# Kernel tuning notes

Hardware: AMD Instinct MI355X
Metric: run time of the kernel (lower is better)

Reference implementation:

```python
import jax, jax.numpy as jnp
import numpy as np

N, M, D = 16384, 8192, 3
ATOM_DIMS, CHEM, K = 6, 16, 16
GAMMA = 1.0
BIG = 1e10


def _leaky(x):
    return jax.nn.leaky_relu(x, negative_slope=0.2)


def _linear(x, W, b=None):
    # torch nn.Linear: y = x @ W.T + b, W: [out, in]
    y = x @ W.T
    return y if b is None else y + b


def setup_inputs() -> dict:
    key = jax.random.key(0)
    ks = jax.random.split(key, 16)

    def lin(k, out_d, in_d):
        bound = 1.0 / np.sqrt(in_d)
        k1, k2 = jax.random.split(k)
        W = jax.random.uniform(k1, (out_d, in_d), minval=-bound, maxval=bound, dtype=jnp.float32)
        b = jax.random.uniform(k2, (out_d,), minval=-bound, maxval=bound, dtype=jnp.float32)
        return W, b

    W_t1, b_t1 = lin(ks[0], CHEM, ATOM_DIMS)
    W_t2, b_t2 = lin(ks[1], CHEM, CHEM)
    W_t3, b_t3 = lin(ks[2], CHEM, CHEM)
    W_att = jax.random.uniform(ks[3], (1, K), minval=-1.0 / np.sqrt(K), maxval=1.0 / np.sqrt(K), dtype=jnp.float32)
    W_e1, b_e1 = lin(ks[4], CHEM, CHEM)
    W_e2, b_e2 = lin(ks[5], CHEM, CHEM)
    W_e3, b_e3 = lin(ks[6], CHEM, CHEM)

    return {
        "xyz": jax.random.normal(ks[7], (N, D), dtype=jnp.float32) * 10.0,
        "atom_xyz": jax.random.normal(ks[8], (M, D), dtype=jnp.float32) * 10.0,
        "atomtypes": jax.random.uniform(ks[9], (M, ATOM_DIMS), dtype=jnp.float32),
        "batch": jnp.zeros((N,), dtype=jnp.int64),
        "atom_batch": jnp.zeros((M,), dtype=jnp.int64),
        "W_t1": W_t1, "b_t1": b_t1, "W_t2": W_t2, "b_t2": b_t2, "W_t3": W_t3, "b_t3": b_t3,
        "W_att": W_att,
        "W_e1": W_e1, "b_e1": b_e1, "W_e2": W_e2, "b_e2": b_e2, "W_e3": W_e3, "b_e3": b_e3,
    }


def reference(xyz, atom_xyz, atomtypes, batch, atom_batch,
              W_t1, b_t1, W_t2, b_t2, W_t3, b_t3, W_att,
              W_e1, b_e1, W_e2, b_e2, W_e3, b_e3):
    # transform_types MLP on atom one-hots -> [M, CHEM]
    t = atomtypes[:, :ATOM_DIMS]
    t = _leaky(_linear(t, W_t1, b_t1))
    t = _leaky(_linear(t, W_t2, b_t2))
    t = _leaky(_linear(t, W_t3, b_t3))

    # batched kNN: squared distances [N, M], cross-batch pairs masked out
    d2 = (jnp.sum(xyz * xyz, -1)[:, None] + jnp.sum(atom_xyz * atom_xyz, -1)[None, :]
          - 2.0 * (xyz @ atom_xyz.T))
    d2 = jnp.where(batch[:, None] == atom_batch[None, :], d2, BIG)
    _, idx = jax.lax.top_k(-d2, K)  # idx: [N, K] nearest atoms

    x_ik = atom_xyz[idx]                       # [N, K, 3]
    vecs = xyz[:, None, :] - x_ik              # [N, K, 3]
    dists = jnp.sum(vecs * vecs, -1)           # [N, K]
    w = jnp.power(dists + 1e-8, -(1.0 + GAMMA) / 2.0)
    norm_vec = vecs * w[:, :, None]            # [N, K, 3]
    feat = t[idx]                              # [N, K, CHEM]

    # outer product [N, K, 3, C] transposed to [N, C, 3, K], attention Linear over K,
    # fused into one einsum (dropout is identity at eval)
    fx = jnp.einsum('nkd,nkc,k->ncd', norm_vec, feat, W_att[0])  # [N, C, 3]
    fx = jnp.sqrt(jnp.sum(fx * fx, -1))        # [N, C]

    fx = _leaky(_linear(fx, W_e1, b_e1))
    fx = _leaky(_linear(fx, W_e2, b_e2))
    fx = _linear(fx, W_e3, b_e3)
    return fx
```

## Files before the change

kernel.cpp:

```cpp
#include <hip/hip_runtime.h>
#include <cfloat>

#define NPTS   16384
#define MATOMS 8192
#define CH     16
#define ADIM   6
#define KNN    16
#define GROUPS_PER_BLOCK 8
#define BIGF   1e10f
#define SLOTS  16
#define CHUNK  512
#define NCHUNK (MATOMS/CHUNK)
#define VMINC  4
#define NPASS  (VMINC + NCHUNK)

__device__ __forceinline__ float leakyf(float x) { return x >= 0.0f ? x : 0.2f * x; }

__global__ void __launch_bounds__(256) prep_kernel(
    const float* __restrict__ atom_xyz,
    const float* __restrict__ atomtypes,
    const int*   __restrict__ atom_batch,
    const float* __restrict__ Wt1, const float* __restrict__ bt1,
    const float* __restrict__ Wt2, const float* __restrict__ bt2,
    const float* __restrict__ Wt3, const float* __restrict__ bt3,
    float4* __restrict__ pos4,
    float*  __restrict__ tbuf,
    int*    __restrict__ abatch)
{
    __shared__ float w1[CH*ADIM], w2[CH*CH], w3[CH*CH], bb1[CH], bb2[CH], bb3[CH];
    const int tid = threadIdx.x;
    if (tid < CH*ADIM) w1[tid] = Wt1[tid];
    if (tid < CH*CH)   { w2[tid] = Wt2[tid]; w3[tid] = Wt3[tid]; }
    if (tid < CH)      { bb1[tid] = bt1[tid]; bb2[tid] = bt2[tid]; bb3[tid] = bt3[tid]; }
    __syncthreads();
    const int m = blockIdx.x * 256 + tid;
    if (m >= MATOMS) return;

    float x[ADIM];
    #pragma unroll
    for (int j = 0; j < ADIM; ++j) x[j] = atomtypes[m*ADIM + j];

    float h0[CH], h1[CH], h2[CH];
    #pragma unroll
    for (int c = 0; c < CH; ++c) {
        float a = 0.0f;
        #pragma unroll
        for (int j = 0; j < ADIM; ++j) a = fmaf(w1[c*ADIM+j], x[j], a);
        h0[c] = leakyf(a + bb1[c]);
    }
    #pragma unroll
    for (int c = 0; c < CH; ++c) {
        float a = 0.0f;
        #pragma unroll
        for (int j = 0; j < CH; ++j) a = fmaf(w2[c*CH+j], h0[j], a);
        h1[c] = leakyf(a + bb2[c]);
    }
    #pragma unroll
    for (int c = 0; c < CH; ++c) {
        float a = 0.0f;
        #pragma unroll
        for (int j = 0; j < CH; ++j) a = fmaf(w3[c*CH+j], h1[j], a);
        h2[c] = leakyf(a + bb3[c]);
    }
    #pragma unroll
    for (int c = 0; c < CH; ++c) tbuf[m*CH + c] = h2[c];

    const float ax = atom_xyz[m*3+0], ay = atom_xyz[m*3+1], az = atom_xyz[m*3+2];
    const float a2 = __fadd_rn(__fadd_rn(__fmul_rn(ax,ax), __fmul_rn(ay,ay)), __fmul_rn(az,az));
    pos4[m] = make_float4(ax, ay, az, a2);
    abatch[m] = atom_batch[m];
}

__global__ void __launch_bounds__(256) atom_main_kernel(
    const float* __restrict__ xyz,
    const int*   __restrict__ batch,
    const float4* __restrict__ pos4,
    const float* __restrict__ tbuf,
    const int*   __restrict__ abatch,
    const float* __restrict__ Watt,
    const float* __restrict__ We1, const float* __restrict__ be1,
    const float* __restrict__ We2, const float* __restrict__ be2,
    const float* __restrict__ We3, const float* __restrict__ be3,
    float* __restrict__ out)
{
    __shared__ float lw1t[CH*CH], lw2t[CH*CH], lw3t[CH*CH];
    __shared__ float lb1[CH], lb2[CH], lb3[CH], lwatt[KNN];
    __shared__ unsigned short lbuf[GROUPS_PER_BLOCK * SLOTS * 32];
    __shared__ float4 lpos[2][CHUNK];
    __shared__ int    lbat[2][CHUNK];
    const int tid = threadIdx.x;
    lw1t[tid] = We1[(tid & 15)*CH + (tid >> 4)];
    lw2t[tid] = We2[(tid & 15)*CH + (tid >> 4)];
    lw3t[tid] = We3[(tid & 15)*CH + (tid >> 4)];
    if (tid < CH) { lb1[tid] = be1[tid]; lb2[tid] = be2[tid]; lb3[tid] = be3[tid]; lwatt[tid] = Watt[tid]; }

    const int c32 = tid & 31;
    const int grp = tid >> 5;
    const int n   = blockIdx.x * GROUPS_PER_BLOCK + grp;

    const float px = xyz[n*3+0], py = xyz[n*3+1], pz = xyz[n*3+2];
    const float pn2 = __fadd_rn(__fadd_rn(__fmul_rn(px,px), __fmul_rn(py,py)), __fmul_rn(pz,pz));
    const int pb = batch[n];

    {
        const float4 q0 = pos4[tid];
        const float4 q1 = pos4[tid+256];
        const int    e0 = abatch[tid];
        const int    e1 = abatch[tid+256];
        lpos[0][tid] = q0; lpos[0][tid+256] = q1;
        lbat[0][tid] = e0; lbat[0][tid+256] = e1;
    }

    float vmin = FLT_MAX;
    float tauf = 0.0f;
    int   skip = 0;
    int   cnt  = 0;
    unsigned short* seg = &lbuf[grp * (SLOTS*32) + c32];

    for (int g = 0; g < NPASS; ++g) {
        const int cur = g & 1;
        __syncthreads();
        float4 q0, q1; int e0, e1;
        const bool pf = (g+1 < NPASS);
        if (pf) {
            const int nc = (g+1 < VMINC) ? (g+1) : (g+1-VMINC);
            const int base = nc*CHUNK;
            q0 = pos4[base+tid]; q1 = pos4[base+tid+256];
            e0 = abatch[base+tid]; e1 = abatch[base+tid+256];
        }
        if (g == VMINC) {
            float tau = FLT_MAX;
            float v = vmin;
            #pragma unroll
            for (int k = 0; k < KNN; ++k) {
                float d = v;
                d = fminf(d, __shfl_xor(d, 1));
                d = fminf(d, __shfl_xor(d, 2));
                d = fminf(d, __shfl_xor(d, 4));
                d = fminf(d, __shfl_xor(d, 8));
                d = fminf(d, __shfl_xor(d, 16));
                tau = d;
                if (v == d) v = FLT_MAX;
            }
            skip = !(tau < BIGF);
            tauf = tau + (1e-5f*(fabsf(pn2) + fabsf(tau)) + 1e-2f);
        }
        if (g < VMINC) {
            #pragma unroll 4
            for (int t = 0; t < CHUNK/32; ++t) {
                const int il = t*32 + c32;
                const float4 a = lpos[cur][il];
                const float dot = fmaf(pz, a.z, fmaf(py, a.y, __fmul_rn(px, a.x)));
                const float lhs = fmaf(-2.0f, dot, a.w);
                if (lhs < vmin) { if (lbat[cur][il] == pb) vmin = lhs; }
            }
        } else if (!skip) {
            const int cb = g - VMINC;
            #pragma unroll 4
            for (int t = 0; t < CHUNK/32; ++t) {
                const int il = t*32 + c32;
                const float4 a = lpos[cur][il];
                const float dot = fmaf(pz, a.z, fmaf(py, a.y, __fmul_rn(px, a.x)));
                const float lhs = fmaf(-2.0f, dot, a.w);
                if (lhs <= tauf) {
                    if (lbat[cur][il] == pb) {
                        const int gi = cb*CHUNK + il;
                        if (cnt < SLOTS) seg[cnt*32] = (unsigned short)gi;
                        ++cnt;
                    }
                }
            }
        }
        if (pf) {
            lpos[cur^1][tid] = q0; lpos[cur^1][tid+256] = q1;
            lbat[cur^1][tid] = e0; lbat[cur^1][tid+256] = e1;
        }
    }

    int ovf = skip | (cnt > SLOTS);
    ovf |= __shfl_xor(ovf, 1);
    ovf |= __shfl_xor(ovf, 2);
    ovf |= __shfl_xor(ovf, 4);
    ovf |= __shfl_xor(ovf, 8);
    ovf |= __shfl_xor(ovf, 16);

    float bd[KNN]; int bi[KNN];
    #pragma unroll
    for (int j = 0; j < KNN; ++j) { bd[j] = FLT_MAX; bi[j] = 0x7fffffff; }

    if (ovf) {
        for (int t = 0; t < MATOMS/32; ++t) {
            const int i = t*32 + c32;
            const float4 a = pos4[i];
            const int ab = abatch[i];
            const float dot = fmaf(pz, a.z, fmaf(py, a.y, __fmul_rn(px, a.x)));
            float d2 = __fsub_rn(__fadd_rn(pn2, a.w), 2.0f * dot);
            d2 = (ab == pb) ? d2 : BIGF;
            if (d2 < bd[KNN-1]) {
                float d = d2; int id = i;
                #pragma unroll
                for (int j = 0; j < KNN; ++j) {
                    const bool sw = d < bd[j];
                    const float od = bd[j]; const int oi = bi[j];
                    bd[j] = sw ? d  : bd[j];
                    bi[j] = sw ? id : bi[j];
                    d  = sw ? od : d;
                    id = sw ? oi : id;
                }
            }
        }
    } else {
        for (int s = 0; s < cnt; ++s) {
            const int i = (int)seg[s*32];
            const float4 a = pos4[i];
            const float dot = fmaf(pz, a.z, fmaf(py, a.y, __fmul_rn(px, a.x)));
            const float d2 = __fsub_rn(__fadd_rn(pn2, a.w), 2.0f * dot);
            if (d2 < bd[KNN-1]) {
                float d = d2; int id = i;
                #pragma unroll
                for (int j = 0; j < KNN; ++j) {
                    const bool sw = d < bd[j];
                    const float od = bd[j]; const int oi = bi[j];
                    bd[j] = sw ? d  : bd[j];
                    bi[j] = sw ? id : bi[j];
                    d  = sw ? od : d;
                    id = sw ? oi : id;
                }
            }
        }
    }

    int idxk[KNN];
    #pragma unroll
    for (int k = 0; k < KNN; ++k) {
        float d = bd[0]; int i = bi[0];
        #pragma unroll
        for (int m = 1; m <= 16; m <<= 1) {
            const float pd = __shfl_xor(d, m);
            const int   pi = __shfl_xor(i, m);
            const bool take = (pd < d) || (pd == d && pi < i);
            d = take ? pd : d;
            i = take ? pi : i;
        }
        idxk[k] = i;
        const bool win = (bd[0] == d) && (bi[0] == i);
        if (win) {
            #pragma unroll
            for (int j = 0; j < KNN-1; ++j) { bd[j] = bd[j+1]; bi[j] = bi[j+1]; }
            bd[KNN-1] = FLT_MAX; bi[KNN-1] = 0x7fffffff;
        }
    }

    if ((tid & 16) == 0) {
        const int c = tid & 15;
        float ac0 = 0.0f, ac1 = 0.0f, ac2 = 0.0f;
        #pragma unroll
        for (int k = 0; k < KNN; ++k) {
            const int j = idxk[k];
            const float4 a = pos4[j];
            const float v0 = __fsub_rn(px, a.x);
            const float v1 = __fsub_rn(py, a.y);
            const float v2 = __fsub_rn(pz, a.z);
            const float dist = __fadd_rn(__fadd_rn(__fmul_rn(v0,v0), __fmul_rn(v1,v1)), __fmul_rn(v2,v2));
            const float w = 1.0f / __fadd_rn(dist, 1e-8f);
            const float nv0 = __fmul_rn(v0, w);
            const float nv1 = __fmul_rn(v1, w);
            const float nv2 = __fmul_rn(v2, w);
            const float fc = tbuf[(size_t)j * CH + c];
            const float fw = __fmul_rn(fc, lwatt[k]);
            ac0 = fmaf(nv0, fw, ac0);
            ac1 = fmaf(nv1, fw, ac1);
            ac2 = fmaf(nv2, fw, ac2);
        }
        const float s = __fadd_rn(__fadd_rn(__fmul_rn(ac0,ac0), __fmul_rn(ac1,ac1)),
                                  __fmul_rn(ac2,ac2));
        const float fx = sqrtf(s);

        float a1 = 0.0f;
        #pragma unroll
        for (int j = 0; j < CH; ++j) {
            const float fj = __shfl(fx, j, 16);
            a1 = fmaf(lw1t[j*CH + c], fj, a1);
        }
        const float g1 = leakyf(a1 + lb1[c]);

        float a2 = 0.0f;
        #pragma unroll
        for (int j = 0; j < CH; ++j) {
            const float gj = __shfl(g1, j, 16);
            a2 = fmaf(lw2t[j*CH + c], gj, a2);
        }
        const float g2 = leakyf(a2 + lb2[c]);

        float a3 = 0.0f;
        #pragma unroll
        for (int j = 0; j < CH; ++j) {
            const float gj = __shfl(g2, j, 16);
            a3 = fmaf(lw3t[j*CH + c], gj, a3);
        }
        out[(size_t)n*CH + c] = a3 + lb3[c];
    }
}

extern "C" void kernel_launch(void* const* d_in, const int* in_sizes, int n_in,
                              void* d_out, int out_size, void* d_ws, size_t ws_size,
                              hipStream_t stream)
{
    (void)in_sizes; (void)n_in; (void)out_size; (void)ws_size;
    const float* xyz        = (const float*)d_in[0];
    const float* atom_xyz   = (const float*)d_in[1];
    const float* atomtypes  = (const float*)d_in[2];
    const int*   batch      = (const int*)d_in[3];
    const int*   atom_batch = (const int*)d_in[4];
    const float* Wt1 = (const float*)d_in[5];
    const float* bt1 = (const float*)d_in[6];
    const float* Wt2 = (const float*)d_in[7];
    const float* bt2 = (const float*)d_in[8];
    const float* Wt3 = (const float*)d_in[9];
    const float* bt3 = (const float*)d_in[10];
    const float* Watt = (const float*)d_in[11];
    const float* We1 = (const float*)d_in[12];
    const float* be1 = (const float*)d_in[13];
    const float* We2 = (const float*)d_in[14];
    const float* be2 = (const float*)d_in[15];
    const float* We3 = (const float*)d_in[16];
    const float* be3 = (const float*)d_in[17];

    char* ws = (char*)d_ws;
    float4* pos4  = (float4*)ws;
    float*  tbuf  = (float*)(ws + 131072);
    int*    abat  = (int*)(ws + 131072 + 524288);
    float*  out   = (float*)d_out;

    hipLaunchKernelGGL(prep_kernel, dim3(MATOMS/256), dim3(256), 0, stream,
                       atom_xyz, atomtypes, atom_batch,
                       Wt1, bt1, Wt2, bt2, Wt3, bt3,
                       pos4, tbuf, abat);
    hipLaunchKernelGGL(atom_main_kernel, dim3(NPTS/GROUPS_PER_BLOCK), dim3(256), 0, stream,
                       xyz, batch, pos4, tbuf, abat,
                       Watt, We1, be1, We2, be2, We3, be3,
                       out);
}
```

Measured before the change: 132.6 us.

## Sample strided atoms for kNN threshold and share per-group candidate list

The threshold estimate now comes from a strided sample of 1024 atoms read straight from global memory, replacing the four shared-memory warm-up chunks. Candidates under the threshold go into one per-group shared list via shared atomics instead of per-lane 16-slot buffers, and lanes then process that list round-robin. The batch check moves from the scan to the final top-k insertion, which drops the staged batch arrays. This removes passes and shared-memory traffic and balances candidate work across lanes, at the cost of shared atomic contention and a possibly looser threshold, since the list admits candidates from other batches.

```diff
diff --git a/kernel.cpp b/kernel.cpp
--- a/kernel.cpp
+++ b/kernel.cpp
@@ -8,11 +8,9 @@
 #define KNN    16
 #define GROUPS_PER_BLOCK 8
 #define BIGF   1e10f
-#define SLOTS  16
+#define GSLOTS 384
 #define CHUNK  512
 #define NCHUNK (MATOMS/CHUNK)
-#define VMINC  4
-#define NPASS  (VMINC + NCHUNK)
 
 __device__ __forceinline__ float leakyf(float x) { return x >= 0.0f ? x : 0.2f * x; }
 
@@ -85,14 +83,15 @@
 {
     __shared__ float lw1t[CH*CH], lw2t[CH*CH], lw3t[CH*CH];
     __shared__ float lb1[CH], lb2[CH], lb3[CH], lwatt[KNN];
-    __shared__ unsigned short lbuf[GROUPS_PER_BLOCK * SLOTS * 32];
+    __shared__ unsigned short gseg[GROUPS_PER_BLOCK][GSLOTS];
+    __shared__ int gcnt[GROUPS_PER_BLOCK];
     __shared__ float4 lpos[2][CHUNK];
-    __shared__ int    lbat[2][CHUNK];
     const int tid = threadIdx.x;
     lw1t[tid] = We1[(tid & 15)*CH + (tid >> 4)];
     lw2t[tid] = We2[(tid & 15)*CH + (tid >> 4)];
     lw3t[tid] = We3[(tid & 15)*CH + (tid >> 4)];
     if (tid < CH) { lb1[tid] = be1[tid]; lb2[tid] = be2[tid]; lb3[tid] = be3[tid]; lwatt[tid] = Watt[tid]; }
+    if (tid < GROUPS_PER_BLOCK) gcnt[tid] = 0;
 
     const int c32 = tid & 31;
     const int grp = tid >> 5;
@@ -105,57 +104,52 @@
     {
         const float4 q0 = pos4[tid];
         const float4 q1 = pos4[tid+256];
-        const int    e0 = abatch[tid];
-        const int    e1 = abatch[tid+256];
         lpos[0][tid] = q0; lpos[0][tid+256] = q1;
-        lbat[0][tid] = e0; lbat[0][tid+256] = e1;
     }
 
     float vmin = FLT_MAX;
-    float tauf = 0.0f;
-    int   skip = 0;
-    int   cnt  = 0;
-    unsigned short* seg = &lbuf[grp * (SLOTS*32) + c32];
-
-    for (int g = 0; g < NPASS; ++g) {
+    for (int t4 = 0; t4 < 8; ++t4) {
+        float4 A[4];
+        #pragma unroll
+        for (int u = 0; u < 4; ++u) A[u] = pos4[((t4*4 + u)*32 + c32) * 8];
+        #pragma unroll
+        for (int u = 0; u < 4; ++u) {
+            const float dot = fmaf(pz, A[u].z, fmaf(py, A[u].y, __fmul_rn(px, A[u].x)));
+            const float lhs = fmaf(-2.0f, dot, A[u].w);
+            if (lhs < vmin) {
+                if (abatch[((t4*4 + u)*32 + c32) * 8] == pb) vmin = lhs;
+            }
+        }
+    }
+
+    float tau = FLT_MAX;
+    {
+        float v = vmin;
+        #pragma unroll
+        for (int k = 0; k < KNN; ++k) {
+            float d = v;
+            d = fminf(d, __shfl_xor(d, 1));
+            d = fminf(d, __shfl_xor(d, 2));
+            d = fminf(d, __shfl_xor(d, 4));
+            d = fminf(d, __shfl_xor(d, 8));
+            d = fminf(d, __shfl_xor(d, 16));
+            tau = d;
+            if (v == d) v = FLT_MAX;
+        }
+    }
+    const int skip = !(tau < BIGF);
+    const float tauf = tau + (1e-5f*(fabsf(pn2) + fabsf(tau)) + 1e-2f);
+
+    for (int g = 0; g < NCHUNK; ++g) {
         const int cur = g & 1;
         __syncthreads();
-        float4 q0, q1; int e0, e1;
-        const bool pf = (g+1 < NPASS);
+        float4 q0, q1;
+        const bool pf = (g+1 < NCHUNK);
         if (pf) {
-            const int nc = (g+1 < VMINC) ? (g+1) : (g+1-VMINC);
-            const int base = nc*CHUNK;
+            const int base = (g+1)*CHUNK;
             q0 = pos4[base+tid]; q1 = pos4[base+tid+256];
-            e0 = abatch[base+tid]; e1 = abatch[base+tid+256];
-        }
-        if (g == VMINC) {
-            float tau = FLT_MAX;
-            float v = vmin;
-            #pragma unroll
-            for (int k = 0; k < KNN; ++k) {
-                float d = v;
-                d = fminf(d, __shfl_xor(d, 1));
-                d = fminf(d, __shfl_xor(d, 2));
-                d = fminf(d, __shfl_xor(d, 4));
-                d = fminf(d, __shfl_xor(d, 8));
-                d = fminf(d, __shfl_xor(d, 16));
-                tau = d;
-                if (v == d) v = FLT_MAX;
-            }
-            skip = !(tau < BIGF);
-            tauf = tau + (1e-5f*(fabsf(pn2) + fabsf(tau)) + 1e-2f);
-        }
-        if (g < VMINC) {
-            #pragma unroll 4
-            for (int t = 0; t < CHUNK/32; ++t) {
-                const int il = t*32 + c32;
-                const float4 a = lpos[cur][il];
-                const float dot = fmaf(pz, a.z, fmaf(py, a.y, __fmul_rn(px, a.x)));
-                const float lhs = fmaf(-2.0f, dot, a.w);
-                if (lhs < vmin) { if (lbat[cur][il] == pb) vmin = lhs; }
-            }
-        } else if (!skip) {
-            const int cb = g - VMINC;
+        }
+        if (!skip) {
             #pragma unroll 4
             for (int t = 0; t < CHUNK/32; ++t) {
                 const int il = t*32 + c32;
@@ -163,26 +157,18 @@
                 const float dot = fmaf(pz, a.z, fmaf(py, a.y, __fmul_rn(px, a.x)));
                 const float lhs = fmaf(-2.0f, dot, a.w);
                 if (lhs <= tauf) {
-                    if (lbat[cur][il] == pb) {
-                        const int gi = cb*CHUNK + il;
-                        if (cnt < SLOTS) seg[cnt*32] = (unsigned short)gi;
-                        ++cnt;
-                    }
+                    const int slot = atomicAdd(&gcnt[grp], 1);
+                    if (slot < GSLOTS) gseg[grp][slot] = (unsigned short)(g*CHUNK + il);
                 }
             }
         }
         if (pf) {
             lpos[cur^1][tid] = q0; lpos[cur^1][tid+256] = q1;
-            lbat[cur^1][tid] = e0; lbat[cur^1][tid+256] = e1;
-        }
-    }
-
-    int ovf = skip | (cnt > SLOTS);
-    ovf |= __shfl_xor(ovf, 1);
-    ovf |= __shfl_xor(ovf, 2);
-    ovf |= __shfl_xor(ovf, 4);
-    ovf |= __shfl_xor(ovf, 8);
-    ovf |= __shfl_xor(ovf, 16);
+        }
+    }
+
+    const int cnt = gcnt[grp];
+    const int ovf = skip | (cnt > GSLOTS);
 
     float bd[KNN]; int bi[KNN];
     #pragma unroll
@@ -210,16 +196,16 @@
             }
         }
     } else {
-        for (int s = 0; s < cnt; ++s) {
-            const int i = (int)seg[s*32];
+        for (int s = c32; s < cnt; s += 32) {
+            const int i = (int)gseg[grp][s];
             const float4 a = pos4[i];
             const float dot = fmaf(pz, a.z, fmaf(py, a.y, __fmul_rn(px, a.x)));
             const float d2 = __fsub_rn(__fadd_rn(pn2, a.w), 2.0f * dot);
-            if (d2 < bd[KNN-1]) {
+            if (abatch[i] == pb) {
                 float d = d2; int id = i;
                 #pragma unroll
                 for (int j = 0; j < KNN; ++j) {
-                    const bool sw = d < bd[j];
+                    const bool sw = (d < bd[j]) || (d == bd[j] && id < bi[j]);
                     const float od = bd[j]; const int oi = bi[j];
                     bd[j] = sw ? d  : bd[j];
                     bi[j] = sw ? id : bi[j];
```

After: 160.3 us. 1.21x slower.

## Halve staging chunk, drop shared batch array, defer batch check to candidates

Applied to the files above, without the earlier changes.

Shrinks the shared-memory atom staging chunk from 512 to 256 and stops staging atom batch ids in shared memory. The batch id is now read from global memory only when a candidate passes the distance test, and for the collected candidates it is checked in the final insertion step, which also gains index-based tie breaking. The goal is less shared-memory traffic and footprint per pass, possibly better occupancy. In exchange there are twice as many synchronized passes and scattered global loads inside the vmin scan. Candidates from other batches now fill slots, so overflow to the slow full-scan fallback can happen more often.

```diff
diff --git a/kernel.cpp b/kernel.cpp
--- a/kernel.cpp
+++ b/kernel.cpp
@@ -9,9 +9,9 @@
 #define GROUPS_PER_BLOCK 8
 #define BIGF   1e10f
 #define SLOTS  16
-#define CHUNK  512
+#define CHUNK  256
 #define NCHUNK (MATOMS/CHUNK)
-#define VMINC  4
+#define VMINC  8
 #define NPASS  (VMINC + NCHUNK)
 
 __device__ __forceinline__ float leakyf(float x) { return x >= 0.0f ? x : 0.2f * x; }
@@ -87,7 +87,6 @@
     __shared__ float lb1[CH], lb2[CH], lb3[CH], lwatt[KNN];
     __shared__ unsigned short lbuf[GROUPS_PER_BLOCK * SLOTS * 32];
     __shared__ float4 lpos[2][CHUNK];
-    __shared__ int    lbat[2][CHUNK];
     const int tid = threadIdx.x;
     lw1t[tid] = We1[(tid & 15)*CH + (tid >> 4)];
     lw2t[tid] = We2[(tid & 15)*CH + (tid >> 4)];
@@ -102,14 +101,7 @@
     const float pn2 = __fadd_rn(__fadd_rn(__fmul_rn(px,px), __fmul_rn(py,py)), __fmul_rn(pz,pz));
     const int pb = batch[n];
 
-    {
-        const float4 q0 = pos4[tid];
-        const float4 q1 = pos4[tid+256];
-        const int    e0 = abatch[tid];
-        const int    e1 = abatch[tid+256];
-        lpos[0][tid] = q0; lpos[0][tid+256] = q1;
-        lbat[0][tid] = e0; lbat[0][tid+256] = e1;
-    }
+    if (tid < CHUNK) lpos[0][tid] = pos4[tid];
 
     float vmin = FLT_MAX;
     float tauf = 0.0f;
@@ -120,13 +112,11 @@
     for (int g = 0; g < NPASS; ++g) {
         const int cur = g & 1;
         __syncthreads();
-        float4 q0, q1; int e0, e1;
-        const bool pf = (g+1 < NPASS);
+        float4 q0;
+        const bool pf = (g+1 < NPASS) && (tid < CHUNK);
         if (pf) {
             const int nc = (g+1 < VMINC) ? (g+1) : (g+1-VMINC);
-            const int base = nc*CHUNK;
-            q0 = pos4[base+tid]; q1 = pos4[base+tid+256];
-            e0 = abatch[base+tid]; e1 = abatch[base+tid+256];
+            q0 = pos4[nc*CHUNK + tid];
         }
         if (g == VMINC) {
             float tau = FLT_MAX;
@@ -152,7 +142,9 @@
                 const float4 a = lpos[cur][il];
                 const float dot = fmaf(pz, a.z, fmaf(py, a.y, __fmul_rn(px, a.x)));
                 const float lhs = fmaf(-2.0f, dot, a.w);
-                if (lhs < vmin) { if (lbat[cur][il] == pb) vmin = lhs; }
+                if (lhs < vmin) {
+                    if (abatch[g*CHUNK + il] == pb) vmin = lhs;
+                }
             }
         } else if (!skip) {
             const int cb = g - VMINC;
@@ -163,17 +155,14 @@
                 const float dot = fmaf(pz, a.z, fmaf(py, a.y, __fmul_rn(px, a.x)));
                 const float lhs = fmaf(-2.0f, dot, a.w);
                 if (lhs <= tauf) {
-                    if (lbat[cur][il] == pb) {
-                        const int gi = cb*CHUNK + il;
-                        if (cnt < SLOTS) seg[cnt*32] = (unsigned short)gi;
-                        ++cnt;
-                    }
+                    const int gi = cb*CHUNK + il;
+                    if (cnt < SLOTS) seg[cnt*32] = (unsigned short)gi;
+                    ++cnt;
                 }
             }
         }
         if (pf) {
-            lpos[cur^1][tid] = q0; lpos[cur^1][tid+256] = q1;
-            lbat[cur^1][tid] = e0; lbat[cur^1][tid+256] = e1;
+            lpos[cur^1][tid] = q0;
         }
     }
 
@@ -210,16 +199,17 @@
             }
         }
     } else {
-        for (int s = 0; s < cnt; ++s) {
+        const int nc = cnt;
+        for (int s = 0; s < nc; ++s) {
             const int i = (int)seg[s*32];
             const float4 a = pos4[i];
             const float dot = fmaf(pz, a.z, fmaf(py, a.y, __fmul_rn(px, a.x)));
             const float d2 = __fsub_rn(__fadd_rn(pn2, a.w), 2.0f * dot);
-            if (d2 < bd[KNN-1]) {
+            if (abatch[i] == pb && d2 <= bd[KNN-1]) {
                 float d = d2; int id = i;
                 #pragma unroll
                 for (int j = 0; j < KNN; ++j) {
-                    const bool sw = d < bd[j];
+                    const bool sw = (d < bd[j]) || (d == bd[j] && id < bi[j]);
                     const float od = bd[j]; const int oi = bi[j];
                     bd[j] = sw ? d  : bd[j];
                     bi[j] = sw ? id : bi[j];
```

Measured after the change: 144.4 us. +8.9%, slower.

## Process two query points per 32-lane group to reuse staged atom tiles

Applied to the files above, without the earlier changes.

Each 32-lane group now handles two query points, so every atom position staged in shared memory is reused for two distance evaluations, and the grid is halved. The batch-id shared staging is removed: batch checks move out of the candidate-collection loop and into the final refinement, which now also breaks distance ties by index. The epilogue uses both 16-lane halves of the group, one per point, for the feature accumulation and MLP. This raises register pressure and the number of candidate slots in shared memory, and halves the number of blocks available to fill the GPU.

```diff
diff --git a/kernel.cpp b/kernel.cpp
--- a/kernel.cpp
+++ b/kernel.cpp
@@ -7,6 +7,7 @@
 #define ADIM   6
 #define KNN    16
 #define GROUPS_PER_BLOCK 8
+#define PTSPG  2
 #define BIGF   1e10f
 #define SLOTS  16
 #define CHUNK  512
@@ -71,112 +72,12 @@
     abatch[m] = atom_batch[m];
 }
 
-__global__ void __launch_bounds__(256) atom_main_kernel(
-    const float* __restrict__ xyz,
-    const int*   __restrict__ batch,
-    const float4* __restrict__ pos4,
-    const float* __restrict__ tbuf,
-    const int*   __restrict__ abatch,
-    const float* __restrict__ Watt,
-    const float* __restrict__ We1, const float* __restrict__ be1,
-    const float* __restrict__ We2, const float* __restrict__ be2,
-    const float* __restrict__ We3, const float* __restrict__ be3,
-    float* __restrict__ out)
+__device__ __forceinline__ void knn_tail(
+    int c32, float px, float py, float pz, float pn2, int pb,
+    int skip, int cnt, const unsigned short* seg,
+    const float4* __restrict__ pos4, const int* __restrict__ abatch,
+    int* idxk)
 {
-    __shared__ float lw1t[CH*CH], lw2t[CH*CH], lw3t[CH*CH];
-    __shared__ float lb1[CH], lb2[CH], lb3[CH], lwatt[KNN];
-    __shared__ unsigned short lbuf[GROUPS_PER_BLOCK * SLOTS * 32];
-    __shared__ float4 lpos[2][CHUNK];
-    __shared__ int    lbat[2][CHUNK];
-    const int tid = threadIdx.x;
-    lw1t[tid] = We1[(tid & 15)*CH + (tid >> 4)];
-    lw2t[tid] = We2[(tid & 15)*CH + (tid >> 4)];
-    lw3t[tid] = We3[(tid & 15)*CH + (tid >> 4)];
-    if (tid < CH) { lb1[tid] = be1[tid]; lb2[tid] = be2[tid]; lb3[tid] = be3[tid]; lwatt[tid] = Watt[tid]; }
-
-    const int c32 = tid & 31;
-    const int grp = tid >> 5;
-    const int n   = blockIdx.x * GROUPS_PER_BLOCK + grp;
-
-    const float px = xyz[n*3+0], py = xyz[n*3+1], pz = xyz[n*3+2];
-    const float pn2 = __fadd_rn(__fadd_rn(__fmul_rn(px,px), __fmul_rn(py,py)), __fmul_rn(pz,pz));
-    const int pb = batch[n];
-
-    {
-        const float4 q0 = pos4[tid];
-        const float4 q1 = pos4[tid+256];
-        const int    e0 = abatch[tid];
-        const int    e1 = abatch[tid+256];
-        lpos[0][tid] = q0; lpos[0][tid+256] = q1;
-        lbat[0][tid] = e0; lbat[0][tid+256] = e1;
-    }
-
-    float vmin = FLT_MAX;
-    float tauf = 0.0f;
-    int   skip = 0;
-    int   cnt  = 0;
-    unsigned short* seg = &lbuf[grp * (SLOTS*32) + c32];
-
-    for (int g = 0; g < NPASS; ++g) {
-        const int cur = g & 1;
-        __syncthreads();
-        float4 q0, q1; int e0, e1;
-        const bool pf = (g+1 < NPASS);
-        if (pf) {
-            const int nc = (g+1 < VMINC) ? (g+1) : (g+1-VMINC);
-            const int base = nc*CHUNK;
-            q0 = pos4[base+tid]; q1 = pos4[base+tid+256];
-            e0 = abatch[base+tid]; e1 = abatch[base+tid+256];
-        }
-        if (g == VMINC) {
-            float tau = FLT_MAX;
-            float v = vmin;
-            #pragma unroll
-            for (int k = 0; k < KNN; ++k) {
-                float d = v;
-                d = fminf(d, __shfl_xor(d, 1));
-                d = fminf(d, __shfl_xor(d, 2));
-                d = fminf(d, __shfl_xor(d, 4));
-                d = fminf(d, __shfl_xor(d, 8));
-                d = fminf(d, __shfl_xor(d, 16));
-                tau = d;
-                if (v == d) v = FLT_MAX;
-            }
-            skip = !(tau < BIGF);
-            tauf = tau + (1e-5f*(fabsf(pn2) + fabsf(tau)) + 1e-2f);
-        }
-        if (g < VMINC) {
-            #pragma unroll 4
-            for (int t = 0; t < CHUNK/32; ++t) {
-                const int il = t*32 + c32;
-                const float4 a = lpos[cur][il];
-                const float dot = fmaf(pz, a.z, fmaf(py, a.y, __fmul_rn(px, a.x)));
-                const float lhs = fmaf(-2.0f, dot, a.w);
-                if (lhs < vmin) { if (lbat[cur][il] == pb) vmin = lhs; }
-            }
-        } else if (!skip) {
-            const int cb = g - VMINC;
-            #pragma unroll 4
-            for (int t = 0; t < CHUNK/32; ++t) {
-                const int il = t*32 + c32;
-                const float4 a = lpos[cur][il];
-                const float dot = fmaf(pz, a.z, fmaf(py, a.y, __fmul_rn(px, a.x)));
-                const float lhs = fmaf(-2.0f, dot, a.w);
-                if (lhs <= tauf) {
-                    if (lbat[cur][il] == pb) {
-                        const int gi = cb*CHUNK + il;
-                        if (cnt < SLOTS) seg[cnt*32] = (unsigned short)gi;
-                        ++cnt;
-                    }
-                }
-            }
-        }
-        if (pf) {
-            lpos[cur^1][tid] = q0; lpos[cur^1][tid+256] = q1;
-            lbat[cur^1][tid] = e0; lbat[cur^1][tid+256] = e1;
-        }
-    }
-
     int ovf = skip | (cnt > SLOTS);
     ovf |= __shfl_xor(ovf, 1);
     ovf |= __shfl_xor(ovf, 2);
@@ -215,11 +116,11 @@
             const float4 a = pos4[i];
             const float dot = fmaf(pz, a.z, fmaf(py, a.y, __fmul_rn(px, a.x)));
             const float d2 = __fsub_rn(__fadd_rn(pn2, a.w), 2.0f * dot);
-            if (d2 < bd[KNN-1]) {
+            if (abatch[i] == pb && d2 <= bd[KNN-1]) {
                 float d = d2; int id = i;
                 #pragma unroll
                 for (int j = 0; j < KNN; ++j) {
-                    const bool sw = d < bd[j];
+                    const bool sw = (d < bd[j]) || (d == bd[j] && id < bi[j]);
                     const float od = bd[j]; const int oi = bi[j];
                     bd[j] = sw ? d  : bd[j];
                     bi[j] = sw ? id : bi[j];
@@ -230,7 +131,6 @@
         }
     }
 
-    int idxk[KNN];
     #pragma unroll
     for (int k = 0; k < KNN; ++k) {
         float d = bd[0]; int i = bi[0];
@@ -250,13 +150,157 @@
             bd[KNN-1] = FLT_MAX; bi[KNN-1] = 0x7fffffff;
         }
     }
-
-    if ((tid & 16) == 0) {
+}
+
+__global__ void __launch_bounds__(256) atom_main_kernel(
+    const float* __restrict__ xyz,
+    const int*   __restrict__ batch,
+    const float4* __restrict__ pos4,
+    const float* __restrict__ tbuf,
+    const int*   __restrict__ abatch,
+    const float* __restrict__ Watt,
+    const float* __restrict__ We1, const float* __restrict__ be1,
+    const float* __restrict__ We2, const float* __restrict__ be2,
+    const float* __restrict__ We3, const float* __restrict__ be3,
+    float* __restrict__ out)
+{
+    __shared__ float lw1t[CH*CH], lw2t[CH*CH], lw3t[CH*CH];
+    __shared__ float lb1[CH], lb2[CH], lb3[CH], lwatt[KNN];
+    __shared__ unsigned short lbuf[GROUPS_PER_BLOCK * PTSPG * SLOTS * 32];
+    __shared__ float4 lpos[2][CHUNK];
+    const int tid = threadIdx.x;
+    lw1t[tid] = We1[(tid & 15)*CH + (tid >> 4)];
+    lw2t[tid] = We2[(tid & 15)*CH + (tid >> 4)];
+    lw3t[tid] = We3[(tid & 15)*CH + (tid >> 4)];
+    if (tid < CH) { lb1[tid] = be1[tid]; lb2[tid] = be2[tid]; lb3[tid] = be3[tid]; lwatt[tid] = Watt[tid]; }
+
+    const int c32 = tid & 31;
+    const int grp = tid >> 5;
+    const int n0  = (blockIdx.x * GROUPS_PER_BLOCK + grp) * PTSPG;
+    const int n1  = n0 + 1;
+
+    const float px0 = xyz[n0*3+0], py0 = xyz[n0*3+1], pz0 = xyz[n0*3+2];
+    const float px1 = xyz[n1*3+0], py1 = xyz[n1*3+1], pz1 = xyz[n1*3+2];
+    const float pn20 = __fadd_rn(__fadd_rn(__fmul_rn(px0,px0), __fmul_rn(py0,py0)), __fmul_rn(pz0,pz0));
+    const float pn21 = __fadd_rn(__fadd_rn(__fmul_rn(px1,px1), __fmul_rn(py1,py1)), __fmul_rn(pz1,pz1));
+    const int pb0 = batch[n0];
+    const int pb1 = batch[n1];
+
+    {
+        const float4 q0 = pos4[tid];
+        const float4 q1 = pos4[tid+256];
+        lpos[0][tid] = q0; lpos[0][tid+256] = q1;
+    }
+
+    float vmin0 = FLT_MAX, vmin1 = FLT_MAX;
+    float tauf0 = 0.0f, tauf1 = 0.0f;
+    int   skip0 = 0, skip1 = 0;
+    int   cnt0 = 0, cnt1 = 0;
+    unsigned short* seg0 = &lbuf[(grp*PTSPG + 0) * (SLOTS*32) + c32];
+    unsigned short* seg1 = &lbuf[(grp*PTSPG + 1) * (SLOTS*32) + c32];
+
+    for (int g = 0; g < NPASS; ++g) {
+        const int cur = g & 1;
+        __syncthreads();
+        float4 q0, q1;
+        const bool pf = (g+1 < NPASS);
+        if (pf) {
+            const int nc = (g+1 < VMINC) ? (g+1) : (g+1-VMINC);
+            const int base = nc*CHUNK;
+            q0 = pos4[base+tid]; q1 = pos4[base+tid+256];
+        }
+        if (g == VMINC) {
+            float tau0 = FLT_MAX, tau1 = FLT_MAX;
+            {
+                float v = vmin0;
+                #pragma unroll
+                for (int k = 0; k < KNN; ++k) {
+                    float d = v;
+                    d = fminf(d, __shfl_xor(d, 1));
+                    d = fminf(d, __shfl_xor(d, 2));
+                    d = fminf(d, __shfl_xor(d, 4));
+                    d = fminf(d, __shfl_xor(d, 8));
+                    d = fminf(d, __shfl_xor(d, 16));
+                    tau0 = d;
+                    if (v == d) v = FLT_MAX;
+                }
+            }
+            {
+                float v = vmin1;
+                #pragma unroll
+                for (int k = 0; k < KNN; ++k) {
+                    float d = v;
+                    d = fminf(d, __shfl_xor(d, 1));
+                    d = fminf(d, __shfl_xor(d, 2));
+                    d = fminf(d, __shfl_xor(d, 4));
+                    d = fminf(d, __shfl_xor(d, 8));
+                    d = fminf(d, __shfl_xor(d, 16));
+                    tau1 = d;
+                    if (v == d) v = FLT_MAX;
+                }
+            }
+            skip0 = !(tau0 < BIGF);
+            skip1 = !(tau1 < BIGF);
+            tauf0 = skip0 ? -FLT_MAX : tau0 + (1e-5f*(fabsf(pn20) + fabsf(tau0)) + 1e-2f);
+            tauf1 = skip1 ? -FLT_MAX : tau1 + (1e-5f*(fabsf(pn21) + fabsf(tau1)) + 1e-2f);
+        }
+        if (g < VMINC) {
+            #pragma unroll 4
+            for (int t = 0; t < CHUNK/32; ++t) {
+                const int il = t*32 + c32;
+                const float4 a = lpos[cur][il];
+                const float dot0 = fmaf(pz0, a.z, fmaf(py0, a.y, __fmul_rn(px0, a.x)));
+                const float lhs0 = fmaf(-2.0f, dot0, a.w);
+                const float dot1 = fmaf(pz1, a.z, fmaf(py1, a.y, __fmul_rn(px1, a.x)));
+                const float lhs1 = fmaf(-2.0f, dot1, a.w);
+                if (lhs0 < vmin0) { if (abatch[g*CHUNK + il] == pb0) vmin0 = lhs0; }
+                if (lhs1 < vmin1) { if (abatch[g*CHUNK + il] == pb1) vmin1 = lhs1; }
+            }
+        } else {
+            const int cb = g - VMINC;
+            #pragma unroll 4
+            for (int t = 0; t < CHUNK/32; ++t) {
+                const int il = t*32 + c32;
+                const float4 a = lpos[cur][il];
+                const float dot0 = fmaf(pz0, a.z, fmaf(py0, a.y, __fmul_rn(px0, a.x)));
+                const float lhs0 = fmaf(-2.0f, dot0, a.w);
+                const float dot1 = fmaf(pz1, a.z, fmaf(py1, a.y, __fmul_rn(px1, a.x)));
+                const float lhs1 = fmaf(-2.0f, dot1, a.w);
+                const int gi = cb*CHUNK + il;
+                if (lhs0 <= tauf0) {
+                    if (cnt0 < SLOTS) seg0[cnt0*32] = (unsigned short)gi;
+                    ++cnt0;
+                }
+                if (lhs1 <= tauf1) {
+                    if (cnt1 < SLOTS) seg1[cnt1*32] = (unsigned short)gi;
+                    ++cnt1;
+                }
+            }
+        }
+        if (pf) {
+            lpos[cur^1][tid] = q0; lpos[cur^1][tid+256] = q1;
+        }
+    }
+
+    int idxk0[KNN], idxk1[KNN];
+    knn_tail(c32, px0, py0, pz0, pn20, pb0, skip0, cnt0, seg0, pos4, abatch, idxk0);
+    knn_tail(c32, px1, py1, pz1, pn21, pb1, skip1, cnt1, seg1, pos4, abatch, idxk1);
+
+    {
+        const int half = (tid >> 4) & 1;
         const int c = tid & 15;
+        const int myn = half ? n1 : n0;
+        const float px = half ? px1 : px0;
+        const float py = half ? py1 : py0;
+        const float pz = half ? pz1 : pz0;
+        int myidx[KNN];
+        #pragma unroll
+        for (int k = 0; k < KNN; ++k) myidx[k] = half ? idxk1[k] : idxk0[k];
+
         float ac0 = 0.0f, ac1 = 0.0f, ac2 = 0.0f;
         #pragma unroll
         for (int k = 0; k < KNN; ++k) {
-            const int j = idxk[k];
+            const int j = myidx[k];
             const float4 a = pos4[j];
             const float v0 = __fsub_rn(px, a.x);
             const float v1 = __fsub_rn(py, a.y);
@@ -298,7 +342,7 @@
             const float gj = __shfl(g2, j, 16);
             a3 = fmaf(lw3t[j*CH + c], gj, a3);
         }
-        out[(size_t)n*CH + c] = a3 + lb3[c];
+        out[(size_t)myn*CH + c] = a3 + lb3[c];
     }
 }
 
@@ -336,7 +380,7 @@
                        atom_xyz, atomtypes, atom_batch,
                        Wt1, bt1, Wt2, bt2, Wt3, bt3,
                        pos4, tbuf, abat);
-    hipLaunchKernelGGL(atom_main_kernel, dim3(NPTS/GROUPS_PER_BLOCK), dim3(256), 0, stream,
+    hipLaunchKernelGGL(atom_main_kernel, dim3(NPTS/(GROUPS_PER_BLOCK*PTSPG)), dim3(256), 0, stream,
                        xyz, batch, pos4, tbuf, abat,
                        Watt, We1, be1, We2, be2, We3, be3,
                        out);
```

Result: faster. 121.9 us (-8.0%).
